# Optimization experiments

Hardware: AMD Instinct MI355X
Metric: run time of the kernel (lower is better)

## Reference

```python
import jax, jax.numpy as jnp
import numpy as np

B, S, H = 64, 1024, 1024

def setup_inputs() -> dict:
    key = jax.random.key(0)
    k1, k2, k3, k4, k5 = jax.random.split(key, 5)
    scale = 1.0 / np.sqrt(H)
    return {
        "decoder_state": jax.random.normal(k1, (B, H), dtype=jnp.float32),
        "encoder_outputs": jax.random.normal(k2, (B, S, H), dtype=jnp.float32),
        "mask": jnp.ones((B, S), dtype=jnp.int32),
        "W_s": jax.random.uniform(k3, (H, H), minval=-scale, maxval=scale, dtype=jnp.float32),
        "W_h": jax.random.uniform(k4, (H, H), minval=-scale, maxval=scale, dtype=jnp.float32),
        "v": jax.random.uniform(k5, (H,), minval=-scale, maxval=scale, dtype=jnp.float32),
    }

def reference(decoder_state, encoder_outputs, mask, W_s, W_h, v):
    # Additive (Bahdanau) attention.
    # proj_s: [B, H] -- original applies W_s to the expanded state (same math, computed once)
    proj_s = decoder_state @ W_s.T
    # proj_h: [B, S, H]
    proj_h = jnp.einsum('bsh,kh->bsk', encoder_outputs, W_h)
    energy = jnp.tanh(proj_s[:, None, :] + proj_h)          # [B, S, H]
    scores = jnp.einsum('bsh,h->bs', energy, v)             # [B, S]
    scores = jnp.where(mask == 0, -jnp.inf, scores)
    weights = jax.nn.softmax(scores, axis=-1)               # [B, S]
    context = jnp.einsum('bs,bsh->bh', weights, encoder_outputs)  # [B, H]
    return context, weights
```

## Files before the change

kernel.cpp:

```cpp
#include <hip/hip_runtime.h>
#include <hip/hip_bf16.h>

#define B_ 64
#define S_ 1024
#define H_ 1024
#define M_ (B_*S_)

typedef __attribute__((ext_vector_type(8))) short short8;
typedef __attribute__((ext_vector_type(4))) float f32x4;

__device__ __forceinline__ unsigned short f2bf(float f) {
    union { float f; unsigned u; } c; c.f = f;
    unsigned u = c.u;
    unsigned r = (u + 0x7fffu + ((u >> 16) & 1u)) >> 16;
    return (unsigned short)r;
}

__device__ __forceinline__ float bf2f(unsigned short h) {
    union { unsigned u; float f; } c; c.u = ((unsigned)h) << 16;
    return c.f;
}

__device__ __forceinline__ float tanh_fast(float x) {
    float t = __expf(2.0f * x);
    return 1.0f - 2.0f * __builtin_amdgcn_rcpf(t + 1.0f);
}

__device__ __forceinline__ void gll16(const unsigned short* g, unsigned short* l) {
    auto* gp = (const __attribute__((address_space(1))) unsigned short*)(g);
    auto* lp = (__attribute__((address_space(3))) unsigned short*)(l);
    __builtin_amdgcn_global_load_lds(gp, lp, 16, 0, 0);
}

__global__ void cvt_bf16_kernel(const float* __restrict__ src,
                                unsigned short* __restrict__ dst, int n8) {
    int idx = blockIdx.x * blockDim.x + threadIdx.x;
    int stride = gridDim.x * blockDim.x;
    for (int i = idx; i < n8; i += stride) {
        const float4* s4 = (const float4*)src + (size_t)i * 2;
        float4 a = s4[0], b = s4[1];
        short8 o;
        o[0] = f2bf(a.x); o[1] = f2bf(a.y); o[2] = f2bf(a.z); o[3] = f2bf(a.w);
        o[4] = f2bf(b.x); o[5] = f2bf(b.y); o[6] = f2bf(b.z); o[7] = f2bf(b.w);
        *((short8*)dst + i) = o;
    }
}

__global__ void proj_s_part_kernel(const float* __restrict__ dec,
                                   const float* __restrict__ Ws,
                                   float* __restrict__ part) {
    __shared__ float wss[64][68];
    const int kt = blockIdx.x & 15, hs = blockIdx.x >> 4;
    const int k0 = kt * 64, h0 = hs * 64;
    const int t = threadIdx.x;

    {
        const int r = t >> 2, c = (t & 3) * 16;
        const float4* src = (const float4*)(Ws + (size_t)(k0 + r) * H_ + h0 + c);
        float4 v0 = src[0], v1 = src[1], v2 = src[2], v3 = src[3];
        *(float4*)&wss[r][c + 0]  = v0;
        *(float4*)&wss[r][c + 4]  = v1;
        *(float4*)&wss[r][c + 8]  = v2;
        *(float4*)&wss[r][c + 12] = v3;
    }
    const int b = t >> 2, kq = t & 3;
    float4 dreg[16];
    const float4* dsrc = (const float4*)(dec + (size_t)b * H_ + h0);
#pragma unroll
    for (int i = 0; i < 16; ++i) dreg[i] = dsrc[i];
    __syncthreads();

    float acc[16] = {};
#pragma unroll
    for (int h4 = 0; h4 < 16; ++h4) {
        float4 d = dreg[h4];
#pragma unroll
        for (int j = 0; j < 16; ++j) {
            float4 wv = *(const float4*)&wss[kq + 4 * j][h4 * 4];
            acc[j] = fmaf(d.x, wv.x, acc[j]);
            acc[j] = fmaf(d.y, wv.y, acc[j]);
            acc[j] = fmaf(d.z, wv.z, acc[j]);
            acc[j] = fmaf(d.w, wv.w, acc[j]);
        }
    }
#pragma unroll
    for (int j = 0; j < 16; ++j)
        part[(size_t)hs * M_ + b * H_ + k0 + kq + 4 * j] = acc[j];
}

__global__ void proj_red_kernel(const float* __restrict__ part,
                                float* __restrict__ proj_s) {
    int i = blockIdx.x * 256 + threadIdx.x;
    float s = 0.0f;
#pragma unroll
    for (int p = 0; p < 16; ++p) s += part[(size_t)p * M_ + i];
    proj_s[i] = s;
}

__global__ void __launch_bounds__(512)
fused_scores_h2_kernel(const unsigned short* __restrict__ encb,
                       const unsigned short* __restrict__ Whb,
                       const float* __restrict__ proj_s,
                       const float* __restrict__ v,
                       float* __restrict__ scores_part) {
    __shared__ __align__(16) unsigned short Lsh[65536];

    const int bx0 = blockIdx.x;
    const int bx = (bx0 & 7) * 128 + (bx0 >> 3);
    const int nt = bx & 3;
    const int mt = bx >> 2;
    const int t = threadIdx.x;
    const int wid = t >> 6, lane = t & 63;
    const int wr = wid >> 2, wc = wid & 3;
    const int lrow = lane & 15, lgrp = lane >> 4;

    f32x4 acc[8][4] = {};

    const int srow = t >> 3;
    const int sgran = (t & 7) ^ (srow & 7);
    const unsigned short* gA = encb + (size_t)(mt * 256 + srow) * H_ + sgran * 8;
    const unsigned short* gB = Whb  + (size_t)(nt * 256 + srow) * H_ + sgran * 8;

#define STG(bb, op, g, kt) \
    gll16(((op) ? gB : gA) + (size_t)(g) * 64 * H_ + (kt) * 64, \
          Lsh + (bb) * 32768 + (op) * 16384 + (g) * 4096 + wid * 512)

    int aoff[8], boff[4];
#pragma unroll
    for (int m = 0; m < 8; ++m) {
        int row = wr * 128 + m * 16 + lrow;
        aoff[m] = row * 64 + (lgrp ^ (row & 7)) * 8;
    }
#pragma unroll
    for (int n = 0; n < 4; ++n) {
        int row = wc * 64 + n * 16 + lrow;
        boff[n] = 16384 + row * 64 + (lgrp ^ (row & 7)) * 8;
    }

    STG(0,1,0,0); STG(0,1,1,0); STG(0,1,2,0); STG(0,1,3,0);
    STG(0,0,0,0); STG(0,0,1,0); STG(0,0,2,0); STG(0,0,3,0);
    asm volatile("s_waitcnt vmcnt(0)" ::: "memory");
    __builtin_amdgcn_sched_barrier(0);
    __builtin_amdgcn_s_barrier();

    int buf = 0;
    for (int s = 0; s < 16; ++s) {
        const int hb = buf * 32768;
        const int sb = buf ^ 1;
        const bool st = (s < 15);
        short8 a0[4], a1[4], bk0[4], bk1[4];

#pragma unroll
        for (int n = 0; n < 4; ++n) bk0[n] = *(const short8*)&Lsh[hb + boff[n]];
#pragma unroll
        for (int n = 0; n < 4; ++n) bk1[n] = *(const short8*)&Lsh[hb + (boff[n] ^ 32)];
#pragma unroll
        for (int m = 0; m < 4; ++m) a0[m] = *(const short8*)&Lsh[hb + aoff[m]];
#pragma unroll
        for (int m = 0; m < 4; ++m) a1[m] = *(const short8*)&Lsh[hb + (aoff[m] ^ 32)];
        if (st) { STG(sb,1,0,s+1); STG(sb,1,1,s+1); STG(sb,1,2,s+1); STG(sb,1,3,s+1); }
        __builtin_amdgcn_s_setprio(1);
#pragma unroll
        for (int m = 0; m < 4; ++m)
#pragma unroll
            for (int n = 0; n < 4; ++n)
                acc[m][n] = __builtin_amdgcn_mfma_f32_16x16x32_bf16(a0[m], bk0[n], acc[m][n], 0, 0, 0);
#pragma unroll
        for (int m = 0; m < 4; ++m)
#pragma unroll
            for (int n = 0; n < 4; ++n)
                acc[m][n] = __builtin_amdgcn_mfma_f32_16x16x32_bf16(a1[m], bk1[n], acc[m][n], 0, 0, 0);
        __builtin_amdgcn_s_setprio(0);

        if (st) { asm volatile("s_waitcnt vmcnt(4)" ::: "memory"); }
        else    { asm volatile("s_waitcnt vmcnt(0)" ::: "memory"); }
        __builtin_amdgcn_sched_barrier(0);
        __builtin_amdgcn_s_barrier();

#pragma unroll
        for (int m = 0; m < 4; ++m) a0[m] = *(const short8*)&Lsh[hb + aoff[4 + m]];
#pragma unroll
        for (int m = 0; m < 4; ++m) a1[m] = *(const short8*)&Lsh[hb + (aoff[4 + m] ^ 32)];
        if (st) { STG(sb,0,0,s+1); STG(sb,0,2,s+1); STG(sb,0,1,s+1); STG(sb,0,3,s+1); }
        __builtin_amdgcn_s_setprio(1);
#pragma unroll
        for (int m = 0; m < 4; ++m)
#pragma unroll
            for (int n = 0; n < 4; ++n)
                acc[4 + m][n] = __builtin_amdgcn_mfma_f32_16x16x32_bf16(a0[m], bk0[n], acc[4 + m][n], 0, 0, 0);
#pragma unroll
        for (int m = 0; m < 4; ++m)
#pragma unroll
            for (int n = 0; n < 4; ++n)
                acc[4 + m][n] = __builtin_amdgcn_mfma_f32_16x16x32_bf16(a1[m], bk1[n], acc[4 + m][n], 0, 0, 0);
        __builtin_amdgcn_s_setprio(0);

        if (st) { asm volatile("s_waitcnt vmcnt(2)" ::: "memory"); }
        __builtin_amdgcn_sched_barrier(0);
        __builtin_amdgcn_s_barrier();
        buf ^= 1;
    }
#undef STG

    const int b = mt >> 2;
    float vv[4], ps[4];
#pragma unroll
    for (int n = 0; n < 4; ++n) {
        int col = nt * 256 + wc * 64 + n * 16 + lrow;
        vv[n] = v[col];
        ps[n] = proj_s[b * H_ + col];
    }
    float* sums = (float*)Lsh;
#pragma unroll
    for (int m = 0; m < 8; ++m) {
#pragma unroll
        for (int j = 0; j < 4; ++j) {
            float s = 0.0f;
#pragma unroll
            for (int n = 0; n < 4; ++n)
                s = fmaf(tanh_fast(acc[m][n][j] + ps[n]), vv[n], s);
            s += __shfl_xor(s, 1, 64);
            s += __shfl_xor(s, 2, 64);
            s += __shfl_xor(s, 4, 64);
            s += __shfl_xor(s, 8, 64);
            if (lrow == 0)
                sums[(wr * 128 + m * 16 + lgrp * 4 + j) * 4 + wc] = s;
        }
    }
    __syncthreads();
    if (t < 256) {
        float r = sums[t * 4 + 0] + sums[t * 4 + 1] + sums[t * 4 + 2] + sums[t * 4 + 3];
        scores_part[(size_t)nt * M_ + mt * 256 + t] = r;
    }
}

__global__ void fused_scores_kernel(const float* __restrict__ enc,
                                    const float* __restrict__ Wh,
                                    const float* __restrict__ proj_s,
                                    const float* __restrict__ v,
                                    float* __restrict__ scores_part) {
    __shared__ __align__(16) unsigned short As[128][40];
    __shared__ __align__(16) unsigned short Bs[128][40];
    __shared__ float sums[128][2];

    const int bx = blockIdx.x;
    const int nt = bx & 7;
    const int mt = bx >> 3;
    const int t = threadIdx.x;
    const int w = t >> 6, lane = t & 63;
    const int wr = w >> 1, wc = w & 1;
    const int lrow = lane & 15, lgrp = lane >> 4;

    f32x4 acc[4][4] = {};

    const int srow = t >> 1;
    const int shalf = t & 1;
    const float* gA = enc + (size_t)(mt * 128 + srow) * H_ + shalf * 16;
    const float* gB = Wh  + (size_t)(nt * 128 + srow) * H_ + shalf * 16;
    unsigned short* lA = &As[srow][shalf * 16];
    unsigned short* lB = &Bs[srow][shalf * 16];

    for (int kt = 0; kt < H_ / 32; ++kt) {
        __syncthreads();
        const float4* a4 = (const float4*)(gA + kt * 32);
        const float4* b4 = (const float4*)(gB + kt * 32);
        union { unsigned short us[16]; uint4 q[2]; } pa, pb;
#pragma unroll
        for (int i = 0; i < 4; ++i) {
            float4 av = a4[i];
            float4 bv = b4[i];
            pa.us[i*4+0] = f2bf(av.x); pa.us[i*4+1] = f2bf(av.y);
            pa.us[i*4+2] = f2bf(av.z); pa.us[i*4+3] = f2bf(av.w);
            pb.us[i*4+0] = f2bf(bv.x); pb.us[i*4+1] = f2bf(bv.y);
            pb.us[i*4+2] = f2bf(bv.z); pb.us[i*4+3] = f2bf(bv.w);
        }
        *(uint4*)(lA)     = pa.q[0];
        *(uint4*)(lA + 8) = pa.q[1];
        *(uint4*)(lB)     = pb.q[0];
        *(uint4*)(lB + 8) = pb.q[1];
        __syncthreads();

        short8 af[4], bf[4];
#pragma unroll
        for (int m = 0; m < 4; ++m)
            af[m] = *(const short8*)&As[wr * 64 + m * 16 + lrow][lgrp * 8];
#pragma unroll
        for (int n = 0; n < 4; ++n)
            bf[n] = *(const short8*)&Bs[wc * 64 + n * 16 + lrow][lgrp * 8];
#pragma unroll
        for (int m = 0; m < 4; ++m)
#pragma unroll
            for (int n = 0; n < 4; ++n)
                acc[m][n] = __builtin_amdgcn_mfma_f32_16x16x32_bf16(af[m], bf[n], acc[m][n], 0, 0, 0);
    }

    const int b = mt >> 3;
    float vv[4], ps[4];
#pragma unroll
    for (int n = 0; n < 4; ++n) {
        int col = nt * 128 + wc * 64 + n * 16 + lrow;
        vv[n] = v[col];
        ps[n] = proj_s[b * H_ + col];
    }
    float rs[4][4];
#pragma unroll
    for (int m = 0; m < 4; ++m) {
#pragma unroll
        for (int j = 0; j < 4; ++j) {
            float s = 0.0f;
#pragma unroll
            for (int n = 0; n < 4; ++n)
                s = fmaf(tanh_fast(acc[m][n][j] + ps[n]), vv[n], s);
            s += __shfl_xor(s, 1, 64);
            s += __shfl_xor(s, 2, 64);
            s += __shfl_xor(s, 4, 64);
            s += __shfl_xor(s, 8, 64);
            rs[m][j] = s;
        }
    }
    if (lrow == 0) {
#pragma unroll
        for (int m = 0; m < 4; ++m)
#pragma unroll
            for (int j = 0; j < 4; ++j)
                sums[wr * 64 + m * 16 + lgrp * 4 + j][wc] = rs[m][j];
    }
    __syncthreads();
    if (t < 128)
        scores_part[(size_t)nt * M_ + mt * 128 + t] = sums[t][0] + sums[t][1];
}

__global__ void softmax_kernel(const float* __restrict__ scores_part,
                               const int* __restrict__ mask,
                               float* __restrict__ weights, int np) {
    const int b = blockIdx.x, t = threadIdx.x;
    __shared__ float red[8];
    float sc[4];
#pragma unroll
    for (int i = 0; i < 4; ++i) {
        int s = t + i * 256;
        float x = 0.0f;
        for (int p = 0; p < np; ++p)
            x += scores_part[(size_t)p * M_ + b * S_ + s];
        if (mask[b * S_ + s] == 0) x = -INFINITY;
        sc[i] = x;
    }
    float mx = fmaxf(fmaxf(sc[0], sc[1]), fmaxf(sc[2], sc[3]));
#pragma unroll
    for (int m = 32; m >= 1; m >>= 1) mx = fmaxf(mx, __shfl_xor(mx, m, 64));
    if ((t & 63) == 0) red[t >> 6] = mx;
    __syncthreads();
    mx = fmaxf(fmaxf(red[0], red[1]), fmaxf(red[2], red[3]));

    float e[4]; float sum = 0.0f;
#pragma unroll
    for (int i = 0; i < 4; ++i) { e[i] = __expf(sc[i] - mx); sum += e[i]; }
#pragma unroll
    for (int m = 32; m >= 1; m >>= 1) sum += __shfl_xor(sum, m, 64);
    if ((t & 63) == 0) red[4 + (t >> 6)] = sum;
    __syncthreads();
    sum = red[4] + red[5] + red[6] + red[7];
    float inv = 1.0f / sum;
#pragma unroll
    for (int i = 0; i < 4; ++i)
        weights[b * S_ + t + i * 256] = e[i] * inv;
}

__global__ void context_part_bf16_kernel(const unsigned short* __restrict__ encb,
                                         const float* __restrict__ weights,
                                         float* __restrict__ ctx_part) {
    const int b = blockIdx.x >> 5;
    const int sc = blockIdx.x & 31;
    const int t = threadIdx.x;
    __shared__ float wv[32];
    if (t < 32) wv[t] = weights[b * S_ + sc * 32 + t];
    __syncthreads();
    const short8* e8 = (const short8*)(encb + (size_t)(b * S_ + sc * 32) * H_) + t;
    float a[8] = {};
#pragma unroll 4
    for (int i = 0; i < 32; ++i) {
        short8 ev = e8[(size_t)i * 128];
        float w = wv[i];
#pragma unroll
        for (int j = 0; j < 8; ++j)
            a[j] = fmaf(w, bf2f((unsigned short)ev[j]), a[j]);
    }
    float* dst = ctx_part + (size_t)sc * M_ + b * H_ + t * 8;
    float4 o0; o0.x = a[0]; o0.y = a[1]; o0.z = a[2]; o0.w = a[3];
    float4 o1; o1.x = a[4]; o1.y = a[5]; o1.z = a[6]; o1.w = a[7];
    *(float4*)dst = o0;
    *(float4*)(dst + 4) = o1;
}

__global__ void context_part_kernel(const float* __restrict__ enc,
                                    const float* __restrict__ weights,
                                    float* __restrict__ ctx_part) {
    const int b = blockIdx.x >> 4;
    const int sc = blockIdx.x & 15;
    const int t = threadIdx.x;
    __shared__ float wv[64];
    if (t < 64) wv[t] = weights[b * S_ + sc * 64 + t];
    __syncthreads();
    const float4* e4 = (const float4*)(enc + (size_t)(b * S_ + sc * 64) * H_) + t;
    float ax = 0.f, ay = 0.f, az = 0.f, aw = 0.f;
#pragma unroll 4
    for (int i = 0; i < 64; ++i) {
        float4 ev = e4[i * 256];
        float wgt = wv[i];
        ax = fmaf(wgt, ev.x, ax);
        ay = fmaf(wgt, ev.y, ay);
        az = fmaf(wgt, ev.z, az);
        aw = fmaf(wgt, ev.w, aw);
    }
    float4 o; o.x = ax; o.y = ay; o.z = az; o.w = aw;
    *((float4*)(ctx_part + (size_t)sc * M_ + b * H_) + t) = o;
}

__global__ void ctx_reduce_kernel(const float* __restrict__ ctx_part,
                                  float* __restrict__ ctx, int np) {
    int idx = blockIdx.x * 256 + threadIdx.x;
    float s = 0.0f;
    for (int p = 0; p < np; ++p) s += ctx_part[(size_t)p * M_ + idx];
    ctx[idx] = s;
}

extern "C" void kernel_launch(void* const* d_in, const int* in_sizes, int n_in,
                              void* d_out, int out_size, void* d_ws, size_t ws_size,
                              hipStream_t stream) {
    const float* dec  = (const float*)d_in[0];
    const float* enc  = (const float*)d_in[1];
    const int*   mask = (const int*)d_in[2];
    const float* Ws   = (const float*)d_in[3];
    const float* Wh   = (const float*)d_in[4];
    const float* v    = (const float*)d_in[5];

    float* out = (float*)d_out;

    float* proj_s      = (float*)d_ws;
    float* proj_part   = proj_s + M_;
    float* scores_part = proj_part + 16 * (size_t)M_;
    float* ctx_part    = scores_part + 8 * (size_t)M_;
    unsigned short* encb = (unsigned short*)(ctx_part + 32 * (size_t)M_);
    unsigned short* Whb  = encb + (size_t)B_ * S_ * H_;

    const size_t need_small = 4ull * (1 + 16 + 8 + 32) * M_;
    const size_t need_big   = need_small + 2ull * ((size_t)B_ * S_ * H_ + (size_t)H_ * H_);

    proj_s_part_kernel<<<256, 256, 0, stream>>>(dec, Ws, proj_part);
    proj_red_kernel<<<256, 256, 0, stream>>>(proj_part, proj_s);

    if (ws_size >= need_big) {
        cvt_bf16_kernel<<<2048, 256, 0, stream>>>(enc, encb, B_ * S_ * H_ / 8);
        cvt_bf16_kernel<<<512, 256, 0, stream>>>(Wh, Whb, H_ * H_ / 8);
        fused_scores_h2_kernel<<<1024, 512, 0, stream>>>(encb, Whb, proj_s, v, scores_part);
        softmax_kernel<<<64, 256, 0, stream>>>(scores_part, mask, out + M_, 4);
        context_part_bf16_kernel<<<2048, 128, 0, stream>>>(encb, out + M_, ctx_part);
        ctx_reduce_kernel<<<256, 256, 0, stream>>>(ctx_part, out, 32);
    } else {
        fused_scores_kernel<<<4096, 256, 0, stream>>>(enc, Wh, proj_s, v, scores_part);
        softmax_kernel<<<64, 256, 0, stream>>>(scores_part, mask, out + M_, 8);
        context_part_kernel<<<1024, 256, 0, stream>>>(enc, out + M_, ctx_part);
        ctx_reduce_kernel<<<256, 256, 0, stream>>>(ctx_part, out, 16);
    }
}
```

Before: 262.2 us.

## Switch scores GEMM to 32x32x16 MFMA, merge bf16 conversions, coarsen context

The main scores GEMM now uses 32x32x16 bf16 MFMA fragments instead of 16x16x32, with new LDS offsets and a reworked epilogue reduction across 32 lanes. The two fp32-to-bf16 conversion launches are merged into one kernel. The context partial kernel handles 64 sequence rows per block instead of 32, which halves the partials that the reduce step has to sum. The larger MFMA shape is meant to cut instruction issue and LDS fragment reads per FLOP, at the cost of a different register and LDS access pattern.

```diff
diff --git a/kernel.cpp b/kernel.cpp
--- a/kernel.cpp
+++ b/kernel.cpp
@@ -8,6 +8,7 @@
 
 typedef __attribute__((ext_vector_type(8))) short short8;
 typedef __attribute__((ext_vector_type(4))) float f32x4;
+typedef __attribute__((ext_vector_type(16))) float f32x16;
 
 __device__ __forceinline__ unsigned short f2bf(float f) {
     union { float f; unsigned u; } c; c.f = f;
@@ -32,17 +33,22 @@
     __builtin_amdgcn_global_load_lds(gp, lp, 16, 0, 0);
 }
 
-__global__ void cvt_bf16_kernel(const float* __restrict__ src,
-                                unsigned short* __restrict__ dst, int n8) {
+__global__ void cvt2_bf16_kernel(const float* __restrict__ s0,
+                                 unsigned short* __restrict__ d0, int n0,
+                                 const float* __restrict__ s1,
+                                 unsigned short* __restrict__ d1, int n1) {
     int idx = blockIdx.x * blockDim.x + threadIdx.x;
     int stride = gridDim.x * blockDim.x;
-    for (int i = idx; i < n8; i += stride) {
-        const float4* s4 = (const float4*)src + (size_t)i * 2;
+    for (int i = idx; i < n0 + n1; i += stride) {
+        const float4* s4;
+        unsigned short* dp;
+        if (i < n0) { s4 = (const float4*)s0 + (size_t)i * 2; dp = d0 + (size_t)i * 8; }
+        else { int j = i - n0; s4 = (const float4*)s1 + (size_t)j * 2; dp = d1 + (size_t)j * 8; }
         float4 a = s4[0], b = s4[1];
         short8 o;
         o[0] = f2bf(a.x); o[1] = f2bf(a.y); o[2] = f2bf(a.z); o[3] = f2bf(a.w);
         o[4] = f2bf(b.x); o[5] = f2bf(b.y); o[6] = f2bf(b.z); o[7] = f2bf(b.w);
-        *((short8*)dst + i) = o;
+        *(short8*)dp = o;
     }
 }
 
@@ -98,11 +104,11 @@
 }
 
 __global__ void __launch_bounds__(512)
-fused_scores_h2_kernel(const unsigned short* __restrict__ encb,
-                       const unsigned short* __restrict__ Whb,
-                       const float* __restrict__ proj_s,
-                       const float* __restrict__ v,
-                       float* __restrict__ scores_part) {
+fused_scores_m32_kernel(const unsigned short* __restrict__ encb,
+                        const unsigned short* __restrict__ Whb,
+                        const float* __restrict__ proj_s,
+                        const float* __restrict__ v,
+                        float* __restrict__ scores_part) {
     __shared__ __align__(16) unsigned short Lsh[65536];
 
     const int bx0 = blockIdx.x;
@@ -112,9 +118,9 @@
     const int t = threadIdx.x;
     const int wid = t >> 6, lane = t & 63;
     const int wr = wid >> 2, wc = wid & 3;
-    const int lrow = lane & 15, lgrp = lane >> 4;
-
-    f32x4 acc[8][4] = {};
+    const int l31 = lane & 31, hi = lane >> 5;
+
+    f32x16 acc[4][2] = {};
 
     const int srow = t >> 3;
     const int sgran = (t & 7) ^ (srow & 7);
@@ -125,16 +131,20 @@
     gll16(((op) ? gB : gA) + (size_t)(g) * 64 * H_ + (kt) * 64, \
           Lsh + (bb) * 32768 + (op) * 16384 + (g) * 4096 + wid * 512)
 
-    int aoff[8], boff[4];
-#pragma unroll
-    for (int m = 0; m < 8; ++m) {
-        int row = wr * 128 + m * 16 + lrow;
-        aoff[m] = row * 64 + (lgrp ^ (row & 7)) * 8;
-    }
-#pragma unroll
-    for (int n = 0; n < 4; ++n) {
-        int row = wc * 64 + n * 16 + lrow;
-        boff[n] = 16384 + row * 64 + (lgrp ^ (row & 7)) * 8;
+    int aoff[4][4], boff[2][4];
+#pragma unroll
+    for (int mf = 0; mf < 4; ++mf) {
+        int row = wr * 128 + mf * 32 + l31;
+#pragma unroll
+        for (int ks = 0; ks < 4; ++ks)
+            aoff[mf][ks] = row * 64 + (((ks * 2 + hi) ^ (row & 7))) * 8;
+    }
+#pragma unroll
+    for (int nf = 0; nf < 2; ++nf) {
+        int row = wc * 64 + nf * 32 + l31;
+#pragma unroll
+        for (int ks = 0; ks < 4; ++ks)
+            boff[nf][ks] = 16384 + row * 64 + (((ks * 2 + hi) ^ (row & 7))) * 8;
     }
 
     STG(0,1,0,0); STG(0,1,1,0); STG(0,1,2,0); STG(0,1,3,0);
@@ -148,28 +158,28 @@
         const int hb = buf * 32768;
         const int sb = buf ^ 1;
         const bool st = (s < 15);
-        short8 a0[4], a1[4], bk0[4], bk1[4];
-
-#pragma unroll
-        for (int n = 0; n < 4; ++n) bk0[n] = *(const short8*)&Lsh[hb + boff[n]];
-#pragma unroll
-        for (int n = 0; n < 4; ++n) bk1[n] = *(const short8*)&Lsh[hb + (boff[n] ^ 32)];
-#pragma unroll
-        for (int m = 0; m < 4; ++m) a0[m] = *(const short8*)&Lsh[hb + aoff[m]];
-#pragma unroll
-        for (int m = 0; m < 4; ++m) a1[m] = *(const short8*)&Lsh[hb + (aoff[m] ^ 32)];
+        short8 af[2][4], bk[2][4];
+
+#pragma unroll
+        for (int nf = 0; nf < 2; ++nf)
+#pragma unroll
+            for (int ks = 0; ks < 4; ++ks)
+                bk[nf][ks] = *(const short8*)&Lsh[hb + boff[nf][ks]];
+#pragma unroll
+        for (int mf = 0; mf < 2; ++mf)
+#pragma unroll
+            for (int ks = 0; ks < 4; ++ks)
+                af[mf][ks] = *(const short8*)&Lsh[hb + aoff[mf][ks]];
         if (st) { STG(sb,1,0,s+1); STG(sb,1,1,s+1); STG(sb,1,2,s+1); STG(sb,1,3,s+1); }
         __builtin_amdgcn_s_setprio(1);
 #pragma unroll
-        for (int m = 0; m < 4; ++m)
-#pragma unroll
-            for (int n = 0; n < 4; ++n)
-                acc[m][n] = __builtin_amdgcn_mfma_f32_16x16x32_bf16(a0[m], bk0[n], acc[m][n], 0, 0, 0);
-#pragma unroll
-        for (int m = 0; m < 4; ++m)
-#pragma unroll
-            for (int n = 0; n < 4; ++n)
-                acc[m][n] = __builtin_amdgcn_mfma_f32_16x16x32_bf16(a1[m], bk1[n], acc[m][n], 0, 0, 0);
+        for (int mf = 0; mf < 2; ++mf)
+#pragma unroll
+            for (int nf = 0; nf < 2; ++nf)
+#pragma unroll
+                for (int ks = 0; ks < 4; ++ks)
+                    acc[mf][nf] = __builtin_amdgcn_mfma_f32_32x32x16_bf16(
+                        af[mf][ks], bk[nf][ks], acc[mf][nf], 0, 0, 0);
         __builtin_amdgcn_s_setprio(0);
 
         if (st) { asm volatile("s_waitcnt vmcnt(4)" ::: "memory"); }
@@ -178,21 +188,20 @@
         __builtin_amdgcn_s_barrier();
 
 #pragma unroll
-        for (int m = 0; m < 4; ++m) a0[m] = *(const short8*)&Lsh[hb + aoff[4 + m]];
-#pragma unroll
-        for (int m = 0; m < 4; ++m) a1[m] = *(const short8*)&Lsh[hb + (aoff[4 + m] ^ 32)];
+        for (int mf = 0; mf < 2; ++mf)
+#pragma unroll
+            for (int ks = 0; ks < 4; ++ks)
+                af[mf][ks] = *(const short8*)&Lsh[hb + aoff[2 + mf][ks]];
         if (st) { STG(sb,0,0,s+1); STG(sb,0,2,s+1); STG(sb,0,1,s+1); STG(sb,0,3,s+1); }
         __builtin_amdgcn_s_setprio(1);
 #pragma unroll
-        for (int m = 0; m < 4; ++m)
-#pragma unroll
-            for (int n = 0; n < 4; ++n)
-                acc[4 + m][n] = __builtin_amdgcn_mfma_f32_16x16x32_bf16(a0[m], bk0[n], acc[4 + m][n], 0, 0, 0);
-#pragma unroll
-        for (int m = 0; m < 4; ++m)
-#pragma unroll
-            for (int n = 0; n < 4; ++n)
-                acc[4 + m][n] = __builtin_amdgcn_mfma_f32_16x16x32_bf16(a1[m], bk1[n], acc[4 + m][n], 0, 0, 0);
+        for (int mf = 0; mf < 2; ++mf)
+#pragma unroll
+            for (int nf = 0; nf < 2; ++nf)
+#pragma unroll
+                for (int ks = 0; ks < 4; ++ks)
+                    acc[2 + mf][nf] = __builtin_amdgcn_mfma_f32_32x32x16_bf16(
+                        af[mf][ks], bk[nf][ks], acc[2 + mf][nf], 0, 0, 0);
         __builtin_amdgcn_s_setprio(0);
 
         if (st) { asm volatile("s_waitcnt vmcnt(2)" ::: "memory"); }
@@ -203,28 +212,29 @@
 #undef STG
 
     const int b = mt >> 2;
-    float vv[4], ps[4];
-#pragma unroll
-    for (int n = 0; n < 4; ++n) {
-        int col = nt * 256 + wc * 64 + n * 16 + lrow;
-        vv[n] = v[col];
-        ps[n] = proj_s[b * H_ + col];
+    float vv[2], ps[2];
+#pragma unroll
+    for (int nf = 0; nf < 2; ++nf) {
+        int col = nt * 256 + wc * 64 + nf * 32 + l31;
+        vv[nf] = v[col];
+        ps[nf] = proj_s[b * H_ + col];
     }
     float* sums = (float*)Lsh;
 #pragma unroll
-    for (int m = 0; m < 8; ++m) {
-#pragma unroll
-        for (int j = 0; j < 4; ++j) {
-            float s = 0.0f;
-#pragma unroll
-            for (int n = 0; n < 4; ++n)
-                s = fmaf(tanh_fast(acc[m][n][j] + ps[n]), vv[n], s);
+    for (int mf = 0; mf < 4; ++mf) {
+#pragma unroll
+        for (int j = 0; j < 16; ++j) {
+            float s = fmaf(tanh_fast(acc[mf][0][j] + ps[0]), vv[0],
+                           tanh_fast(acc[mf][1][j] + ps[1]) * vv[1]);
             s += __shfl_xor(s, 1, 64);
             s += __shfl_xor(s, 2, 64);
             s += __shfl_xor(s, 4, 64);
             s += __shfl_xor(s, 8, 64);
-            if (lrow == 0)
-                sums[(wr * 128 + m * 16 + lgrp * 4 + j) * 4 + wc] = s;
+            s += __shfl_xor(s, 16, 64);
+            if (l31 == 0) {
+                int row = wr * 128 + mf * 32 + (j & 3) + 8 * (j >> 2) + 4 * hi;
+                sums[row * 4 + wc] = s;
+            }
         }
     }
     __syncthreads();
@@ -369,16 +379,16 @@
 __global__ void context_part_bf16_kernel(const unsigned short* __restrict__ encb,
                                          const float* __restrict__ weights,
                                          float* __restrict__ ctx_part) {
-    const int b = blockIdx.x >> 5;
-    const int sc = blockIdx.x & 31;
+    const int b = blockIdx.x >> 4;
+    const int sc = blockIdx.x & 15;
     const int t = threadIdx.x;
-    __shared__ float wv[32];
-    if (t < 32) wv[t] = weights[b * S_ + sc * 32 + t];
-    __syncthreads();
-    const short8* e8 = (const short8*)(encb + (size_t)(b * S_ + sc * 32) * H_) + t;
+    __shared__ float wv[64];
+    if (t < 64) wv[t] = weights[b * S_ + sc * 64 + t];
+    __syncthreads();
+    const short8* e8 = (const short8*)(encb + (size_t)(b * S_ + sc * 64) * H_) + t;
     float a[8] = {};
 #pragma unroll 4
-    for (int i = 0; i < 32; ++i) {
+    for (int i = 0; i < 64; ++i) {
         short8 ev = e8[(size_t)i * 128];
         float w = wv[i];
 #pragma unroll
@@ -450,12 +460,12 @@
     proj_red_kernel<<<256, 256, 0, stream>>>(proj_part, proj_s);
 
     if (ws_size >= need_big) {
-        cvt_bf16_kernel<<<2048, 256, 0, stream>>>(enc, encb, B_ * S_ * H_ / 8);
-        cvt_bf16_kernel<<<512, 256, 0, stream>>>(Wh, Whb, H_ * H_ / 8);
-        fused_scores_h2_kernel<<<1024, 512, 0, stream>>>(encb, Whb, proj_s, v, scores_part);
+        cvt2_bf16_kernel<<<2048, 256, 0, stream>>>(enc, encb, B_ * S_ * H_ / 8,
+                                                   Wh, Whb, H_ * H_ / 8);
+        fused_scores_m32_kernel<<<1024, 512, 0, stream>>>(encb, Whb, proj_s, v, scores_part);
         softmax_kernel<<<64, 256, 0, stream>>>(scores_part, mask, out + M_, 4);
-        context_part_bf16_kernel<<<2048, 128, 0, stream>>>(encb, out + M_, ctx_part);
-        ctx_reduce_kernel<<<256, 256, 0, stream>>>(ctx_part, out, 32);
+        context_part_bf16_kernel<<<1024, 128, 0, stream>>>(encb, out + M_, ctx_part);
+        ctx_reduce_kernel<<<256, 256, 0, stream>>>(ctx_part, out, 16);
     } else {
         fused_scores_kernel<<<4096, 256, 0, stream>>>(enc, Wh, proj_s, v, scores_part);
         softmax_kernel<<<64, 256, 0, stream>>>(scores_part, mask, out + M_, 8);
```

Measured after the change: 300.6 us. 14.7% more time.
